# Kernel tuning notes

Measured on AMD Instinct MI355X. Metric: run time of the kernel, lower is better.

The kernel has to match this reference:

```python
import jax, jax.numpy as jnp
import numpy as np

FS, STRIDE, PAD = 3, 1, 1

def setup_inputs() -> dict:
    key = jax.random.key(0)
    k1, k2, k3 = jax.random.split(key, 3)
    N, C, H, W = 4, 256, 64, 64
    out_C = 256
    x = jax.random.normal(k1, (N, C, H, W), jnp.float32)
    # offset/mask conv params (original inits to 0 -> degenerate; use small random)
    offset_w = jax.random.normal(k2, (FS * FS * 3, C, FS, FS), jnp.float32) * 0.01
    offset_b = jnp.zeros((FS * FS * 3,), jnp.float32)
    # xavier_normal-like scale for dcn weight
    dcn_w = jax.random.normal(k3, (out_C, C, FS, FS), jnp.float32) * (1.0 / np.sqrt(C * FS * FS))
    return {"x": x, "offset_w": offset_w, "offset_b": offset_b, "dcn_w": dcn_w}

def _dcnv2(x, offset_w, offset_b, dcn_w):
    fs, stride, pad = FS, STRIDE, PAD
    N, C, H, W = x.shape
    out_C = dcn_w.shape[0]
    K2 = fs * fs
    om = jax.lax.conv_general_dilated(
        x, offset_w, (stride, stride), [(pad, pad), (pad, pad)],
        dimension_numbers=("NCHW", "OIHW", "NCHW")) + offset_b[None, :, None, None]
    Ho, Wo = om.shape[2], om.shape[3]
    offset = om[:, : 2 * K2].reshape(N, K2, 2, Ho, Wo)
    off_y, off_x = offset[:, :, 0], offset[:, :, 1]            # [N,K2,Ho,Wo]
    mask = jax.nn.sigmoid(om[:, 2 * K2:])                      # [N,K2,Ho,Wo]
    # base sampling grid: ori + kernel tap offset
    ky, kx = jnp.meshgrid(jnp.arange(fs), jnp.arange(fs), indexing="ij")
    ky = ky.reshape(K2).astype(jnp.float32)
    kx = kx.reshape(K2).astype(jnp.float32)
    base_y = (jnp.arange(Ho, dtype=jnp.float32) * stride - pad)[None, :, None] + ky[:, None, None]
    base_x = (jnp.arange(Wo, dtype=jnp.float32) * stride - pad)[None, None, :] + kx[:, None, None]
    h_im = base_y[None] + off_y                                # [N,K2,Ho,Wo]
    w_im = base_x[None] + off_x
    y0 = jnp.floor(h_im)
    x0 = jnp.floor(w_im)
    lh, lw = h_im - y0, w_im - x0
    xf = x.reshape(N, C, H * W)

    def gather(yi, xi):
        valid = (yi >= 0) & (yi <= H - 1) & (xi >= 0) & (xi <= W - 1)
        yc = jnp.clip(yi, 0, H - 1).astype(jnp.int32)
        xc = jnp.clip(xi, 0, W - 1).astype(jnp.int32)
        idx = (yc * W + xc).reshape(N, -1)
        v = jax.vmap(lambda img, ind: img[:, ind])(xf, idx)    # [N,C,K2*Ho*Wo]
        v = v.reshape(N, C, K2, Ho, Wo)
        return v * valid[:, None].astype(x.dtype)

    hh, hw = 1.0 - lh, 1.0 - lw
    sampled = ((hh * hw)[:, None] * gather(y0, x0)
               + (hh * lw)[:, None] * gather(y0, x0 + 1)
               + (lh * hw)[:, None] * gather(y0 + 1, x0)
               + (lh * lw)[:, None] * gather(y0 + 1, x0 + 1))  # [N,C,K2,Ho,Wo]
    sampled = sampled * mask[:, None]
    wk = dcn_w.reshape(out_C, C, K2)
    return jnp.einsum("nckhw,ock->nohw", sampled, wk)

def reference(x, offset_w, offset_b, dcn_w):
    return _dcnv2(x, offset_w, offset_b, dcn_w)
```

## Files before the change

kernel.cpp:

```cpp
#include <hip/hip_runtime.h>
#include <hip/hip_bf16.h>
#include <math.h>

#define NB     4
#define CIN    256
#define HH     64
#define WW     64
#define OUTC   256
#define K2     9
#define KTOT   2304
#define HWSZ   4096
#define NSTEPS 72
#define MTOT   16384


typedef __attribute__((ext_vector_type(4)))  float  floatx4;
typedef __attribute__((ext_vector_type(16))) float  floatx16;
typedef __attribute__((ext_vector_type(8)))  short  short8;
typedef __attribute__((ext_vector_type(4)))  short  short4v;
typedef __attribute__((ext_vector_type(4)))  int    intx4;

__device__ __forceinline__ unsigned short f2bf(float f) {
  union { float f; unsigned u; } v; v.f = f;
  unsigned r = v.u + 0x7FFF + ((v.u >> 16) & 1);
  return (unsigned short)(r >> 16);
}
__device__ __forceinline__ float b2f(unsigned short s) {
  union { unsigned u; float f; } v; v.u = ((unsigned)s) << 16;
  return v.f;
}
__device__ __forceinline__ float lo16f(int u) {
  union { int i; float f; } v; v.i = u << 16; return v.f;
}
__device__ __forceinline__ float hi16f(int u) {
  union { int i; float f; } v; v.i = u & 0xFFFF0000; return v.f;
}
__device__ __forceinline__ unsigned cvt_pk_bf16(float lo, float hi) {
  unsigned r;
  asm("v_cvt_pk_bf16_f32 %0, %1, %2" : "=v"(r) : "v"(lo), "v"(hi));
  return r;
}

__device__ __forceinline__ void pack8(const intx4& c0, const intx4& c1,
                                      const intx4& c2, const intx4& c3,
                                      const float4& w, unsigned short* dst) {
  intx4 o;
#pragma unroll
  for (int jj = 0; jj < 4; ++jj) {
    float v0 = w.x * lo16f(c0[jj]) + w.y * lo16f(c1[jj]) +
               w.z * lo16f(c2[jj]) + w.w * lo16f(c3[jj]);
    float v1 = w.x * hi16f(c0[jj]) + w.y * hi16f(c1[jj]) +
               w.z * hi16f(c2[jj]) + w.w * hi16f(c3[jj]);
    o[jj] = (int)cvt_pk_bf16(v0, v1);
  }
  *(intx4*)dst = o;
}

#define LDS_BARRIER() asm volatile("s_waitcnt lgkmcnt(0)\n\ts_barrier" ::: "memory")

#define WSM_BFRAG   0
#define WSM_B2FRAG  1179648
#define WSM_XT      (1179648 + 147456)
#define WSM_END     (WSM_XT + NB * HWSZ * CIN * 2)
#define WSF_BW      0
#define WSF_B2W     (KTOT * OUTC * 2)
#define WSF_OM      (WSF_B2W + KTOT * 32 * 2)
#define WSF_END     (WSF_OM + NB * 27 * HWSZ * 4)

__global__ __launch_bounds__(256) void prep_main_kernel(
    const float* __restrict__ dcn_w, const float* __restrict__ offw,
    const float* __restrict__ x,
    unsigned short* __restrict__ Bfrag, unsigned short* __restrict__ B2frag,
    unsigned short* __restrict__ xt) {
  int bid = blockIdx.x;
  int tid = threadIdx.x;
  if (bid < 256) {
    __shared__ unsigned short T[64 * 266];
    int img = bid >> 6, h = bid & 63;
    const float* xp = x + (size_t)img * CIN * HWSZ + h * 64;
    int w = tid & 63, cq = tid >> 6;
    for (int cb = 0; cb < 256; cb += 4) {
      int c = cb + cq;
      T[w * 266 + c] = f2bf(xp[(size_t)c * HWSZ + w]);
    }
    __syncthreads();
    int w2 = tid >> 2, cg = (tid & 3) << 6;
    unsigned short* o = xt + ((size_t)(img * 64 + h) * 64 + w2) * 256 + cg;
#pragma unroll
    for (int i = 0; i < 64; i += 8) {
      short8 v = *(short8*)&T[w2 * 266 + cg + i];
      *(short8*)(o + i) = v;
    }
  } else if (bid < 320) {
    __shared__ unsigned short W[4 * KTOT];
    int n0 = (bid - 256) * 4;
#pragma unroll
    for (int r = 0; r < 4; ++r)
      for (int c = tid; c < KTOT; c += 256)
        W[r * KTOT + c] = f2bf(dcn_w[(size_t)(n0 + r) * KTOT + c]);
    __syncthreads();
    for (int i = tid; i < 1152; i += 256) {
      int s16 = i >> 3, hf = (i >> 2) & 1, nl = i & 3;
      int n = n0 + nl;
      int lane = (hf << 5) + (n & 31);
      int e = (((s16 << 3) + (n >> 5)) << 6) + lane;
      int kb = (s16 << 4) + (hf << 3);
      short8 pk;
#pragma unroll
      for (int j = 0; j < 8; ++j) {
        int k = kb + j;
        pk[j] = (short)W[nl * KTOT + (k & 255) * 9 + (k >> 8)];
      }
      *(short8*)(Bfrag + (size_t)e * 8) = pk;
    }
  } else {
    __shared__ unsigned short W2[4 * KTOT];
    int n0 = (bid - 320) * 4;
#pragma unroll
    for (int r = 0; r < 4; ++r) {
      bool ok = (n0 + r) < 27;
      for (int c = tid; c < KTOT; c += 256)
        W2[r * KTOT + c] = ok ? f2bf(offw[(size_t)(n0 + r) * KTOT + c])
                              : (unsigned short)0;
    }
    __syncthreads();
    for (int i = tid; i < 1152; i += 256) {
      int s32 = i >> 4, qq = (i >> 2) & 3, nl = i & 3;
      int n = n0 + nl;
      int lane = (qq << 4) + (n & 15);
      int e = (((s32 << 1) + (n >> 4)) << 6) + lane;
      int kb = (s32 << 5) + (qq << 3);
      short8 pk;
#pragma unroll
      for (int j = 0; j < 8; ++j) {
        int k = kb + j;
        pk[j] = (short)W2[nl * KTOT + (k & 255) * 9 + (k >> 8)];
      }
      *(short8*)(B2frag + (size_t)e * 8) = pk;
    }
  }
}

__global__ __launch_bounds__(512, 2) void dcn_fused_kernel(
    const unsigned short* __restrict__ xt,
    const unsigned short* __restrict__ Bfrag,
    const unsigned short* __restrict__ B2frag,
    const float* __restrict__ ob, float* __restrict__ out) {
  __shared__ unsigned short Ald[4][520 * 8];
  __shared__ intx4  sOff[576];
  __shared__ float4 sWt[576];
  __shared__ float  omp[4 * 32 * 68];

  int braw = blockIdx.x;
  int bid  = ((braw & 7) << 5) + (braw >> 3);
  int img = bid >> 6, h = bid & 63;
  const unsigned short* xb = xt + (size_t)img * HWSZ * 256;

  int tid  = threadIdx.x;
  int lane = tid & 63, q = tid >> 6;
  int quad = lane >> 4, l15 = lane & 15;
  int l31  = lane & 31,  lh5 = lane >> 5;

  if (q < 4) {
    floatx4 cacc[4][2];
#pragma unroll
    for (int mt = 0; mt < 4; ++mt)
#pragma unroll
      for (int nt = 0; nt < 2; ++nt) cacc[mt][nt] = (floatx4){0.f, 0.f, 0.f, 0.f};
    short8 cpa[2][4];
    short8 cpb[2][2];

#define CONV_LOAD(I, SLOT)                                                     \
  {                                                                            \
    int s = q + (I) * 4;                                                       \
    int t = s >> 3;                                                            \
    int dy = t / 3 - 1, dx = t % 3 - 1;                                        \
    int y = h + dy;                                                            \
    int cb0 = ((s & 7) << 5) + (quad << 3);                                    \
    _Pragma("unroll")                                                          \
    for (int mt = 0; mt < 4; ++mt) {                                           \
      int xx = mt * 16 + l15 + dx;                                             \
      short8 v = {0, 0, 0, 0, 0, 0, 0, 0};                                     \
      if (((unsigned)y < 64u) && ((unsigned)xx < 64u))                         \
        v = *(const short8*)(xb + ((y * 64 + xx) << 8) + cb0);                 \
      cpa[SLOT][mt] = v;                                                       \
    }                                                                          \
    _Pragma("unroll")                                                          \
    for (int nt = 0; nt < 2; ++nt)                                             \
      cpb[SLOT][nt] = *(const short8*)(B2frag + (((s * 2 + nt) * 64 + lane) << 3)); \
  }

    CONV_LOAD(0, 0);
#pragma unroll 2
    for (int i = 0; i < 18; ++i) {
      int sl = i & 1;
      if (i < 17) CONV_LOAD(i + 1, sl ^ 1);
#pragma unroll
      for (int mt = 0; mt < 4; ++mt)
#pragma unroll
        for (int nt = 0; nt < 2; ++nt)
          cacc[mt][nt] = __builtin_amdgcn_mfma_f32_16x16x32_bf16(
              cpa[sl][mt], cpb[sl][nt], cacc[mt][nt], 0, 0, 0);
    }
#undef CONV_LOAD
#pragma unroll
    for (int mt = 0; mt < 4; ++mt)
#pragma unroll
      for (int nt = 0; nt < 2; ++nt) {
        int oc = nt * 16 + l15;
        float4 vv = make_float4(cacc[mt][nt][0], cacc[mt][nt][1],
                                cacc[mt][nt][2], cacc[mt][nt][3]);
        *(float4*)&omp[(q * 32 + oc) * 68 + mt * 16 + quad * 4] = vv;
      }
  }
  __syncthreads();

  for (int v = tid; v < 576; v += 512) {
    int w = v & 63, t = v >> 6;
    int ky = t / 3, kx = t % 3;
    float offy = omp[(0 * 32 + 2 * t) * 68 + w] + omp[(1 * 32 + 2 * t) * 68 + w] +
                 omp[(2 * 32 + 2 * t) * 68 + w] + omp[(3 * 32 + 2 * t) * 68 + w] +
                 ob[2 * t];
    float offx = omp[(0 * 32 + 2 * t + 1) * 68 + w] + omp[(1 * 32 + 2 * t + 1) * 68 + w] +
                 omp[(2 * 32 + 2 * t + 1) * 68 + w] + omp[(3 * 32 + 2 * t + 1) * 68 + w] +
                 ob[2 * t + 1];
    float mraw = omp[(0 * 32 + 18 + t) * 68 + w] + omp[(1 * 32 + 18 + t) * 68 + w] +
                 omp[(2 * 32 + 18 + t) * 68 + w] + omp[(3 * 32 + 18 + t) * 68 + w] +
                 ob[18 + t];
    float mv   = 1.0f / (1.0f + __expf(-mraw));
    float him  = (float)(h - 1 + ky) + offy;
    float wim  = (float)(w - 1 + kx) + offx;
    float y0f = floorf(him), x0f = floorf(wim);
    float lhf = him - y0f, lwf = wim - x0f;
    int y0 = (int)y0f, x0i = (int)x0f;
    bool vy0 = (y0 >= 0) && (y0 < HH);
    bool vy1 = (y0 + 1 >= 0) && (y0 + 1 < HH);
    bool vx0 = (x0i >= 0) && (x0i < WW);
    bool vx1 = (x0i + 1 >= 0) && (x0i + 1 < WW);
    float hh_ = 1.0f - lhf, hw_ = 1.0f - lwf;
    float4 wt;
    wt.x = (vy0 && vx0) ? hh_ * hw_ * mv : 0.0f;
    wt.y = (vy0 && vx1) ? hh_ * lwf * mv : 0.0f;
    wt.z = (vy1 && vx0) ? lhf * hw_ * mv : 0.0f;
    wt.w = (vy1 && vx1) ? lhf * lwf * mv : 0.0f;
    int y0c = min(max(y0, 0), 63), y1c = min(max(y0 + 1, 0), 63);
    int x0c = min(max(x0i, 0), 63), x1c = min(max(x0i + 1, 0), 63);
    intx4 ii = {(y0c * 64 + x0c) << 8, (y0c * 64 + x1c) << 8,
                (y1c * 64 + x0c) << 8, (y1c * 64 + x1c) << 8};
    sOff[v] = ii;
    sWt[v]  = wt;
  }

  floatx16 acc[2];
#pragma unroll
  for (int mt = 0; mt < 2; ++mt)
#pragma unroll
    for (int e = 0; e < 16; ++e) acc[mt][e] = 0.f;

  int sm  = tid >> 3;
  int chk = tid & 7;
  int wgran = (((chk >> 1) << 1) + (sm >> 5)) * 65 + ((chk & 1) << 5) + (sm & 31);

  short8 bfr[2][4];
  intx4  cr[2][4];
  float4 pwt[2];

  __syncthreads();

#pragma unroll
  for (int sub = 0; sub < 4; ++sub) {
    bfr[0][sub] = *(const short8*)(
        Bfrag + (((size_t)(0 + sub) * 8 + q) * 64 + lane) * 8);
    bfr[1][sub] = *(const short8*)(
        Bfrag + (((size_t)(4 + sub) * 8 + q) * 64 + lane) * 8);
  }
  {
    intx4 off = sOff[sm];
    float4 w0 = sWt[sm];
    {
      int cb = chk * 8;
      intx4 c0 = *(const intx4*)(xb + off.x + cb);
      intx4 c1 = *(const intx4*)(xb + off.y + cb);
      intx4 c2 = *(const intx4*)(xb + off.z + cb);
      intx4 c3 = *(const intx4*)(xb + off.w + cb);
      pack8(c0, c1, c2, c3, w0, &Ald[0][wgran * 8]);
    }
    {
      int cb = 64 + chk * 8;
      intx4 c0 = *(const intx4*)(xb + off.x + cb);
      intx4 c1 = *(const intx4*)(xb + off.y + cb);
      intx4 c2 = *(const intx4*)(xb + off.z + cb);
      intx4 c3 = *(const intx4*)(xb + off.w + cb);
      pack8(c0, c1, c2, c3, w0, &Ald[1][wgran * 8]);
    }
    {
      int cb = 128 + chk * 8;
      pwt[0] = w0;
      cr[0][0] = *(const intx4*)(xb + off.x + cb);
      cr[0][1] = *(const intx4*)(xb + off.y + cb);
      cr[0][2] = *(const intx4*)(xb + off.z + cb);
      cr[0][3] = *(const intx4*)(xb + off.w + cb);
    }
    {
      int cb = 192 + chk * 8;
      pwt[1] = w0;
      cr[1][0] = *(const intx4*)(xb + off.x + cb);
      cr[1][1] = *(const intx4*)(xb + off.y + cb);
      cr[1][2] = *(const intx4*)(xb + off.z + cb);
      cr[1][3] = *(const intx4*)(xb + off.w + cb);
    }
  }
  LDS_BARRIER();

#pragma unroll 2
  for (int S = 0; S < 18; ++S) {
    int s0 = 2 * S, s1 = s0 + 1;
    __builtin_amdgcn_s_setprio(1);
#pragma unroll
    for (int sub = 0; sub < 4; ++sub) {
      short8 a0 = *(short8*)&Ald[s0 & 3][((sub * 2 + 0) * 65 + lane) * 8];
      short8 a1 = *(short8*)&Ald[s0 & 3][((sub * 2 + 1) * 65 + lane) * 8];
      acc[0] = __builtin_amdgcn_mfma_f32_32x32x16_bf16(
          a0, bfr[0][sub], acc[0], 0, 0, 0);
      acc[1] = __builtin_amdgcn_mfma_f32_32x32x16_bf16(
          a1, bfr[0][sub], acc[1], 0, 0, 0);
    }
    __builtin_amdgcn_s_setprio(0);
    if (s0 + 2 < 36) {
      int s16b = (s0 + 2) * 4;
#pragma unroll
      for (int sub = 0; sub < 4; ++sub)
        bfr[0][sub] = *(const short8*)(
            Bfrag + (((size_t)(s16b + sub) * 8 + q) * 64 + lane) * 8);
      pack8(cr[0][0], cr[0][1], cr[0][2], cr[0][3], pwt[0],
            &Ald[(s0 + 2) & 3][wgran * 8]);
    }
    if (s0 + 4 < 36) {
      int s4 = s0 + 4, t4 = s4 >> 2;
      intx4 off = sOff[t4 * 64 + sm];
      pwt[0] = sWt[t4 * 64 + sm];
      int cb = (s4 & 3) * 64 + chk * 8;
      cr[0][0] = *(const intx4*)(xb + off.x + cb);
      cr[0][1] = *(const intx4*)(xb + off.y + cb);
      cr[0][2] = *(const intx4*)(xb + off.z + cb);
      cr[0][3] = *(const intx4*)(xb + off.w + cb);
    }
    __builtin_amdgcn_s_setprio(1);
#pragma unroll
    for (int sub = 0; sub < 4; ++sub) {
      short8 a0 = *(short8*)&Ald[s1 & 3][((sub * 2 + 0) * 65 + lane) * 8];
      short8 a1 = *(short8*)&Ald[s1 & 3][((sub * 2 + 1) * 65 + lane) * 8];
      acc[0] = __builtin_amdgcn_mfma_f32_32x32x16_bf16(
          a0, bfr[1][sub], acc[0], 0, 0, 0);
      acc[1] = __builtin_amdgcn_mfma_f32_32x32x16_bf16(
          a1, bfr[1][sub], acc[1], 0, 0, 0);
    }
    __builtin_amdgcn_s_setprio(0);
    if (s1 + 2 < 36) {
      int s16b = (s1 + 2) * 4;
#pragma unroll
      for (int sub = 0; sub < 4; ++sub)
        bfr[1][sub] = *(const short8*)(
            Bfrag + (((size_t)(s16b + sub) * 8 + q) * 64 + lane) * 8);
      pack8(cr[1][0], cr[1][1], cr[1][2], cr[1][3], pwt[1],
            &Ald[(s1 + 2) & 3][wgran * 8]);
    }
    if (s1 + 4 < 36) {
      int s4 = s1 + 4, t4 = s4 >> 2;
      intx4 off = sOff[t4 * 64 + sm];
      pwt[1] = sWt[t4 * 64 + sm];
      int cb = (s4 & 3) * 64 + chk * 8;
      cr[1][0] = *(const intx4*)(xb + off.x + cb);
      cr[1][1] = *(const intx4*)(xb + off.y + cb);
      cr[1][2] = *(const intx4*)(xb + off.z + cb);
      cr[1][3] = *(const intx4*)(xb + off.w + cb);
    }
    LDS_BARRIER();
  }

  int oc = q * 32 + l31;
#pragma unroll
  for (int mt = 0; mt < 2; ++mt) {
    float* obase = out + (((size_t)img * OUTC + oc) << 12) + h * 64 +
                   mt * 32 + lh5 * 4;
#pragma unroll
    for (int rg = 0; rg < 4; ++rg) {
      float4 vv = make_float4(acc[mt][rg * 4 + 0], acc[mt][rg * 4 + 1],
                              acc[mt][rg * 4 + 2], acc[mt][rg * 4 + 3]);
      *(float4*)(obase + rg * 8) = vv;
    }
  }
}

__global__ __launch_bounds__(256) void prep_fb_kernel(
    const float* __restrict__ dcn_w, const float* __restrict__ offw,
    unsigned short* __restrict__ Bw, unsigned short* __restrict__ B2w) {
  int oc = blockIdx.x;
  for (int k = threadIdx.x; k < KTOT; k += 256) {
    int t = k >> 8, c = k & 255;
    Bw[oc * KTOT + k] = f2bf(dcn_w[oc * KTOT + c * 9 + t]);
    if (oc < 32)
      B2w[oc * KTOT + k] = (oc < 27) ? f2bf(offw[oc * KTOT + c * 9 + t])
                                     : (unsigned short)0;
  }
}

__global__ __launch_bounds__(256) void conv_offset_kernel(
    const float* __restrict__ x, const unsigned short* __restrict__ B2w,
    const float* __restrict__ ob, float* __restrict__ om) {
  __shared__ unsigned short A_lds[64 * 40];
  __shared__ unsigned short B_lds[32 * 40];
  int bid = blockIdx.x;
  int n = bid >> 6, h = bid & 63;
  int tid = threadIdx.x, lane = tid & 63, q = tid >> 6;
  const float* xn = x + n * (CIN * HWSZ);
  floatx4 acc0 = {0.f, 0.f, 0.f, 0.f}, acc1 = {0.f, 0.f, 0.f, 0.f};
  int w = tid & 63, cg = tid >> 6, ocb = tid >> 3, part = tid & 7;
  for (int s = 0; s < NSTEPS; ++s) {
    int t = s >> 3, c0 = (s & 7) << 5;
    int dy = t / 3 - 1, dx = t % 3 - 1;
    __syncthreads();
    {
      int y = h + dy, xx = w + dx;
      bool inb = ((unsigned)y < 64u) && ((unsigned)xx < 64u);
      const float* xb = xn + (c0 + cg * 8) * HWSZ + y * 64 + xx;
      short8 pk;
#pragma unroll
      for (int j = 0; j < 8; ++j) { float v = inb ? xb[j * HWSZ] : 0.0f; pk[j] = (short)f2bf(v); }
      *(short8*)&A_lds[w * 40 + cg * 8] = pk;
    }
    { const unsigned short* bp = B2w + ocb * KTOT + (t << 8) + c0 + part * 4;
      *(short4v*)&B_lds[ocb * 40 + part * 4] = *(const short4v*)bp; }
    __syncthreads();
    int fr = (lane >> 4) * 8;
    short8 af  = *(short8*)&A_lds[(q * 16 + (lane & 15)) * 40 + fr];
    short8 bf0 = *(short8*)&B_lds[((lane & 15)) * 40 + fr];
    short8 bf1 = *(short8*)&B_lds[(16 + (lane & 15)) * 40 + fr];
    acc0 = __builtin_amdgcn_mfma_f32_16x16x32_bf16(af, bf0, acc0, 0, 0, 0);
    acc1 = __builtin_amdgcn_mfma_f32_16x16x32_bf16(af, bf1, acc1, 0, 0, 0);
  }
  int g = lane >> 4;
#pragma unroll
  for (int nt = 0; nt < 2; ++nt) {
    floatx4 a = nt ? acc1 : acc0;
    int oc = nt * 16 + (lane & 15);
    if (oc < 27) {
      float bias = ob[oc];
#pragma unroll
      for (int r = 0; r < 4; ++r) {
        int wm = q * 16 + g * 4 + r;
        float val = a[r] + bias;
        if (oc >= 18) val = 1.0f / (1.0f + __expf(-val));
        om[((n * 27 + oc) << 12) + h * 64 + wm] = val;
      }
    }
  }
}

__global__ __launch_bounds__(256) void dcn_main_kernel(
    const float* __restrict__ x, const float* __restrict__ om,
    const unsigned short* __restrict__ Bw, float* __restrict__ out) {
  __shared__ unsigned short A_lds[32 * 40];
  __shared__ unsigned short B_lds[256 * 40];
  __shared__ int    sY[288];
  __shared__ int    sX[288];
  __shared__ float4 sW[288];
  int bid = blockIdx.x;
  int n = bid >> 7, rem = bid & 127, h = rem >> 1, w0 = (rem & 1) << 5;
  int tid = threadIdx.x, lane = tid & 63, q = tid >> 6;
  const float* xn  = x + n * (CIN * HWSZ);
  const float* omn = om + n * (27 * HWSZ);
  for (int v = tid; v < 288; v += 256) {
    int m = v & 31, t = v >> 5;
    int ky = t / 3, kx = t % 3;
    int wg = w0 + m, sp = h * 64 + wg;
    float offy = omn[(2 * t) * HWSZ + sp];
    float offx = omn[(2 * t + 1) * HWSZ + sp];
    float mv   = omn[(18 + t) * HWSZ + sp];
    float him = (float)(h - 1 + ky) + offy;
    float wim = (float)(wg - 1 + kx) + offx;
    float y0f = floorf(him), x0f = floorf(wim);
    float lh = him - y0f, lw = wim - x0f;
    int y0 = (int)y0f, x0i = (int)x0f;
    bool vy0 = (y0 >= 0) && (y0 < HH), vy1 = (y0 + 1 >= 0) && (y0 + 1 < HH);
    bool vx0 = (x0i >= 0) && (x0i < WW), vx1 = (x0i + 1 >= 0) && (x0i + 1 < WW);
    float hh_ = 1.0f - lh, hw_ = 1.0f - lw;
    float4 wt;
    wt.x = (vy0 && vx0) ? hh_ * hw_ * mv : 0.0f;
    wt.y = (vy0 && vx1) ? hh_ * lw  * mv : 0.0f;
    wt.z = (vy1 && vx0) ? lh  * hw_ * mv : 0.0f;
    wt.w = (vy1 && vx1) ? lh  * lw  * mv : 0.0f;
    sY[v] = y0; sX[v] = x0i; sW[v] = wt;
  }
  floatx4 acc[2][4];
#pragma unroll
  for (int mi = 0; mi < 2; ++mi)
#pragma unroll
    for (int nj = 0; nj < 4; ++nj) acc[mi][nj] = (floatx4){0.f, 0.f, 0.f, 0.f};
  int m = tid & 31, cg = tid >> 5, n0 = q * 64;
  for (int s = 0; s < NSTEPS; ++s) {
    int t = s >> 3, c0 = (s & 7) << 5;
    __syncthreads();
    {
      int p = t * 32 + m;
      int y0 = sY[p], x0i = sX[p];
      float4 wt = sW[p];
      int y0c = min(max(y0, 0), 63), y1c = min(max(y0 + 1, 0), 63);
      int x0c = min(max(x0i, 0), 63), x1c = min(max(x0i + 1, 0), 63);
      int i00 = y0c * 64 + x0c, i01 = y0c * 64 + x1c;
      int i10 = y1c * 64 + x0c, i11 = y1c * 64 + x1c;
      const float* xb = xn + (c0 + cg * 4) * HWSZ;
      short4v pk;
#pragma unroll
      for (int j = 0; j < 4; ++j) {
        const float* xc = xb + j * HWSZ;
        float v = wt.x * xc[i00] + wt.y * xc[i01] + wt.z * xc[i10] + wt.w * xc[i11];
        pk[j] = (short)f2bf(v);
      }
      *(short4v*)&A_lds[m * 40 + cg * 4] = pk;
    }
    {
      const short8* bp = (const short8*)(Bw + tid * KTOT + (t << 8) + c0);
      short8 b0 = bp[0], b1 = bp[1], b2 = bp[2], b3 = bp[3];
      short8* dst = (short8*)&B_lds[tid * 40];
      dst[0] = b0; dst[1] = b1; dst[2] = b2; dst[3] = b3;
    }
    __syncthreads();
    int fr = (lane >> 4) * 8;
    short8 a0 = *(short8*)&A_lds[((lane & 15)) * 40 + fr];
    short8 a1 = *(short8*)&A_lds[(16 + (lane & 15)) * 40 + fr];
#pragma unroll
    for (int nj = 0; nj < 4; ++nj) {
      short8 bfp = *(short8*)&B_lds[(n0 + nj * 16 + (lane & 15)) * 40 + fr];
      acc[0][nj] = __builtin_amdgcn_mfma_f32_16x16x32_bf16(a0, bfp, acc[0][nj], 0, 0, 0);
      acc[1][nj] = __builtin_amdgcn_mfma_f32_16x16x32_bf16(a1, bfp, acc[1][nj], 0, 0, 0);
    }
  }
  int g = lane >> 4;
#pragma unroll
  for (int mi = 0; mi < 2; ++mi) {
    int wm = w0 + mi * 16 + g * 4;
#pragma unroll
    for (int nj = 0; nj < 4; ++nj) {
      int oc = n0 + nj * 16 + (lane & 15);
      float4 vv = make_float4(acc[mi][nj][0], acc[mi][nj][1],
                              acc[mi][nj][2], acc[mi][nj][3]);
      *(float4*)&out[((n * OUTC + oc) << 12) + h * 64 + wm] = vv;
    }
  }
}

extern "C" void kernel_launch(void* const* d_in, const int* in_sizes, int n_in,
                              void* d_out, int out_size, void* d_ws, size_t ws_size,
                              hipStream_t stream) {
  const float* x     = (const float*)d_in[0];
  const float* offw  = (const float*)d_in[1];
  const float* ob    = (const float*)d_in[2];
  const float* dcn_w = (const float*)d_in[3];
  float* out = (float*)d_out;

  if (ws_size >= (size_t)WSM_END) {
    unsigned short* Bfrag  = (unsigned short*)((char*)d_ws + WSM_BFRAG);
    unsigned short* B2frag = (unsigned short*)((char*)d_ws + WSM_B2FRAG);
    unsigned short* xtb    = (unsigned short*)((char*)d_ws + WSM_XT);
    prep_main_kernel<<<328, 256, 0, stream>>>(dcn_w, offw, x, Bfrag, B2frag, xtb);
    dcn_fused_kernel<<<256, 512, 0, stream>>>(xtb, Bfrag, B2frag, ob, out);
  } else {
    unsigned short* Bw  = (unsigned short*)((char*)d_ws + WSF_BW);
    unsigned short* B2w = (unsigned short*)((char*)d_ws + WSF_B2W);
    float*          omb = (float*)((char*)d_ws + WSF_OM);
    prep_fb_kernel<<<256, 256, 0, stream>>>(dcn_w, offw, Bw, B2w);
    conv_offset_kernel<<<NB * HH, 256, 0, stream>>>(x, B2w, ob, omb);
    dcn_main_kernel<<<NB * HH * 2, 256, 0, stream>>>(x, omb, Bw, out);
  }
}
```

Measured before the change: 130.7 us.

## Split fused DCN blocks into half-row tiles and flatten weight-prep kernel

The fused deformable-conv kernel now processes half an output row (32 pixels) per block instead of a full row, doubling the grid to 512 blocks so every CU gets work and LDS use per block shrinks. Only the first 256 threads produce gathered A tiles, and each wave issues one 32x32 MFMA chain instead of two. The weight-fragment prep drops its LDS staging and has each thread build one fragment straight from global memory over more blocks. The trade-off is that B fragments and the offset-conv halo are loaded twice per row, and half the threads sit idle during packing.

Result: slower. 133.8 us (+2.3%).

```diff
diff --git a/kernel.cpp b/kernel.cpp
--- a/kernel.cpp
+++ b/kernel.cpp
@@ -91,53 +91,31 @@
       short8 v = *(short8*)&T[w2 * 266 + cg + i];
       *(short8*)(o + i) = v;
     }
-  } else if (bid < 320) {
-    __shared__ unsigned short W[4 * KTOT];
-    int n0 = (bid - 256) * 4;
-#pragma unroll
-    for (int r = 0; r < 4; ++r)
-      for (int c = tid; c < KTOT; c += 256)
-        W[r * KTOT + c] = f2bf(dcn_w[(size_t)(n0 + r) * KTOT + c]);
-    __syncthreads();
-    for (int i = tid; i < 1152; i += 256) {
-      int s16 = i >> 3, hf = (i >> 2) & 1, nl = i & 3;
-      int n = n0 + nl;
-      int lane = (hf << 5) + (n & 31);
-      int e = (((s16 << 3) + (n >> 5)) << 6) + lane;
-      int kb = (s16 << 4) + (hf << 3);
-      short8 pk;
-#pragma unroll
-      for (int j = 0; j < 8; ++j) {
-        int k = kb + j;
-        pk[j] = (short)W[nl * KTOT + (k & 255) * 9 + (k >> 8)];
-      }
-      *(short8*)(Bfrag + (size_t)e * 8) = pk;
-    }
+  } else if (bid < 544) {
+    int e = (bid - 256) * 256 + tid;
+    int lane = e & 63, nt = (e >> 6) & 7, s16 = e >> 9;
+    int n = nt * 32 + (lane & 31);
+    int kb = s16 * 16 + ((lane >> 5) << 3);
+    short8 pk;
+#pragma unroll
+    for (int j = 0; j < 8; ++j) {
+      int k = kb + j;
+      pk[j] = (short)f2bf(dcn_w[n * KTOT + (k & 255) * 9 + (k >> 8)]);
+    }
+    *(short8*)(Bfrag + (size_t)e * 8) = pk;
   } else {
-    __shared__ unsigned short W2[4 * KTOT];
-    int n0 = (bid - 320) * 4;
-#pragma unroll
-    for (int r = 0; r < 4; ++r) {
-      bool ok = (n0 + r) < 27;
-      for (int c = tid; c < KTOT; c += 256)
-        W2[r * KTOT + c] = ok ? f2bf(offw[(size_t)(n0 + r) * KTOT + c])
-                              : (unsigned short)0;
-    }
-    __syncthreads();
-    for (int i = tid; i < 1152; i += 256) {
-      int s32 = i >> 4, qq = (i >> 2) & 3, nl = i & 3;
-      int n = n0 + nl;
-      int lane = (qq << 4) + (n & 15);
-      int e = (((s32 << 1) + (n >> 4)) << 6) + lane;
-      int kb = (s32 << 5) + (qq << 3);
-      short8 pk;
-#pragma unroll
-      for (int j = 0; j < 8; ++j) {
-        int k = kb + j;
-        pk[j] = (short)W2[nl * KTOT + (k & 255) * 9 + (k >> 8)];
-      }
-      *(short8*)(B2frag + (size_t)e * 8) = pk;
-    }
+    int e = (bid - 544) * 256 + tid;
+    int lane = e & 63, nt = (e >> 6) & 1, s32 = e >> 7;
+    int n = nt * 16 + (lane & 15);
+    int kb = s32 * 32 + ((lane >> 4) << 3);
+    short8 pk;
+#pragma unroll
+    for (int j = 0; j < 8; ++j) {
+      int k = kb + j;
+      pk[j] = (n < 27) ? (short)f2bf(offw[n * KTOT + (k & 255) * 9 + (k >> 8)])
+                       : (short)0;
+    }
+    *(short8*)(B2frag + (size_t)e * 8) = pk;
   }
 }
 
@@ -146,14 +124,16 @@
     const unsigned short* __restrict__ Bfrag,
     const unsigned short* __restrict__ B2frag,
     const float* __restrict__ ob, float* __restrict__ out) {
-  __shared__ unsigned short Ald[4][520 * 8];
-  __shared__ intx4  sOff[576];
-  __shared__ float4 sWt[576];
-  __shared__ float  omp[4 * 32 * 68];
+  __shared__ unsigned short Ald[4][260 * 8];
+  __shared__ intx4  sOff[288];
+  __shared__ float4 sWt[288];
+  __shared__ float  omp[4 * 32 * 36];
 
   int braw = blockIdx.x;
-  int bid  = ((braw & 7) << 5) + (braw >> 3);
-  int img = bid >> 6, h = bid & 63;
+  int bid  = ((braw & 7) << 6) + (braw >> 3);
+  int rowid = bid >> 1, half = bid & 1;
+  int img = rowid >> 6, h = rowid & 63;
+  int w0 = half << 5;
   const unsigned short* xb = xt + (size_t)img * HWSZ * 256;
 
   int tid  = threadIdx.x;
@@ -162,12 +142,12 @@
   int l31  = lane & 31,  lh5 = lane >> 5;
 
   if (q < 4) {
-    floatx4 cacc[4][2];
-#pragma unroll
-    for (int mt = 0; mt < 4; ++mt)
+    floatx4 cacc[2][2];
+#pragma unroll
+    for (int mt = 0; mt < 2; ++mt)
 #pragma unroll
       for (int nt = 0; nt < 2; ++nt) cacc[mt][nt] = (floatx4){0.f, 0.f, 0.f, 0.f};
-    short8 cpa[2][4];
+    short8 cpa[2][2];
     short8 cpb[2][2];
 
 #define CONV_LOAD(I, SLOT)                                                     \
@@ -178,8 +158,8 @@
     int y = h + dy;                                                            \
     int cb0 = ((s & 7) << 5) + (quad << 3);                                    \
     _Pragma("unroll")                                                          \
-    for (int mt = 0; mt < 4; ++mt) {                                           \
-      int xx = mt * 16 + l15 + dx;                                             \
+    for (int mt = 0; mt < 2; ++mt) {                                           \
+      int xx = w0 + mt * 16 + l15 + dx;                                        \
       short8 v = {0, 0, 0, 0, 0, 0, 0, 0};                                     \
       if (((unsigned)y < 64u) && ((unsigned)xx < 64u))                         \
         v = *(const short8*)(xb + ((y * 64 + xx) << 8) + cb0);                 \
@@ -196,7 +176,7 @@
       int sl = i & 1;
       if (i < 17) CONV_LOAD(i + 1, sl ^ 1);
 #pragma unroll
-      for (int mt = 0; mt < 4; ++mt)
+      for (int mt = 0; mt < 2; ++mt)
 #pragma unroll
         for (int nt = 0; nt < 2; ++nt)
           cacc[mt][nt] = __builtin_amdgcn_mfma_f32_16x16x32_bf16(
@@ -204,32 +184,34 @@
     }
 #undef CONV_LOAD
 #pragma unroll
-    for (int mt = 0; mt < 4; ++mt)
+    for (int mt = 0; mt < 2; ++mt)
 #pragma unroll
       for (int nt = 0; nt < 2; ++nt) {
         int oc = nt * 16 + l15;
         float4 vv = make_float4(cacc[mt][nt][0], cacc[mt][nt][1],
                                 cacc[mt][nt][2], cacc[mt][nt][3]);
-        *(float4*)&omp[(q * 32 + oc) * 68 + mt * 16 + quad * 4] = vv;
+        *(float4*)&omp[(q * 32 + oc) * 36 + mt * 16 + quad * 4] = vv;
       }
   }
   __syncthreads();
 
-  for (int v = tid; v < 576; v += 512) {
-    int w = v & 63, t = v >> 6;
+  if (tid < 288) {
+    int v = tid;
+    int w = v & 31, t = v >> 5;
+    int wg = w0 + w;
     int ky = t / 3, kx = t % 3;
-    float offy = omp[(0 * 32 + 2 * t) * 68 + w] + omp[(1 * 32 + 2 * t) * 68 + w] +
-                 omp[(2 * 32 + 2 * t) * 68 + w] + omp[(3 * 32 + 2 * t) * 68 + w] +
+    float offy = omp[(0 * 32 + 2 * t) * 36 + w] + omp[(1 * 32 + 2 * t) * 36 + w] +
+                 omp[(2 * 32 + 2 * t) * 36 + w] + omp[(3 * 32 + 2 * t) * 36 + w] +
                  ob[2 * t];
-    float offx = omp[(0 * 32 + 2 * t + 1) * 68 + w] + omp[(1 * 32 + 2 * t + 1) * 68 + w] +
-                 omp[(2 * 32 + 2 * t + 1) * 68 + w] + omp[(3 * 32 + 2 * t + 1) * 68 + w] +
+    float offx = omp[(0 * 32 + 2 * t + 1) * 36 + w] + omp[(1 * 32 + 2 * t + 1) * 36 + w] +
+                 omp[(2 * 32 + 2 * t + 1) * 36 + w] + omp[(3 * 32 + 2 * t + 1) * 36 + w] +
                  ob[2 * t + 1];
-    float mraw = omp[(0 * 32 + 18 + t) * 68 + w] + omp[(1 * 32 + 18 + t) * 68 + w] +
-                 omp[(2 * 32 + 18 + t) * 68 + w] + omp[(3 * 32 + 18 + t) * 68 + w] +
+    float mraw = omp[(0 * 32 + 18 + t) * 36 + w] + omp[(1 * 32 + 18 + t) * 36 + w] +
+                 omp[(2 * 32 + 18 + t) * 36 + w] + omp[(3 * 32 + 18 + t) * 36 + w] +
                  ob[18 + t];
     float mv   = 1.0f / (1.0f + __expf(-mraw));
     float him  = (float)(h - 1 + ky) + offy;
-    float wim  = (float)(w - 1 + kx) + offx;
+    float wim  = (float)(wg - 1 + kx) + offx;
     float y0f = floorf(him), x0f = floorf(wim);
     float lhf = him - y0f, lwf = wim - x0f;
     int y0 = (int)y0f, x0i = (int)x0f;
@@ -251,15 +233,14 @@
     sWt[v]  = wt;
   }
 
-  floatx16 acc[2];
-#pragma unroll
-  for (int mt = 0; mt < 2; ++mt)
-#pragma unroll
-    for (int e = 0; e < 16; ++e) acc[mt][e] = 0.f;
-
-  int sm  = tid >> 3;
+  floatx16 acc;
+#pragma unroll
+  for (int e = 0; e < 16; ++e) acc[e] = 0.f;
+
+  int sm  = (tid >> 3) & 31;
   int chk = tid & 7;
-  int wgran = (((chk >> 1) << 1) + (sm >> 5)) * 65 + ((chk & 1) << 5) + (sm & 31);
+  int wgran = (chk >> 1) * 65 + ((chk & 1) << 5) + sm;
+  bool producer = (tid < 256);
 
   short8 bfr[2][4];
   intx4  cr[2][4];
@@ -274,16 +255,16 @@
     bfr[1][sub] = *(const short8*)(
         Bfrag + (((size_t)(4 + sub) * 8 + q) * 64 + lane) * 8);
   }
-  {
+  if (producer) {
     intx4 off = sOff[sm];
-    float4 w0 = sWt[sm];
+    float4 wgt = sWt[sm];
     {
       int cb = chk * 8;
       intx4 c0 = *(const intx4*)(xb + off.x + cb);
       intx4 c1 = *(const intx4*)(xb + off.y + cb);
       intx4 c2 = *(const intx4*)(xb + off.z + cb);
       intx4 c3 = *(const intx4*)(xb + off.w + cb);
-      pack8(c0, c1, c2, c3, w0, &Ald[0][wgran * 8]);
+      pack8(c0, c1, c2, c3, wgt, &Ald[0][wgran * 8]);
     }
     {
       int cb = 64 + chk * 8;
@@ -291,11 +272,11 @@
       intx4 c1 = *(const intx4*)(xb + off.y + cb);
       intx4 c2 = *(const intx4*)(xb + off.z + cb);
       intx4 c3 = *(const intx4*)(xb + off.w + cb);
-      pack8(c0, c1, c2, c3, w0, &Ald[1][wgran * 8]);
+      pack8(c0, c1, c2, c3, wgt, &Ald[1][wgran * 8]);
     }
     {
       int cb = 128 + chk * 8;
-      pwt[0] = w0;
+      pwt[0] = wgt;
       cr[0][0] = *(const intx4*)(xb + off.x + cb);
       cr[0][1] = *(const intx4*)(xb + off.y + cb);
       cr[0][2] = *(const intx4*)(xb + off.z + cb);
@@ -303,7 +284,7 @@
     }
     {
       int cb = 192 + chk * 8;
-      pwt[1] = w0;
+      pwt[1] = wgt;
       cr[1][0] = *(const intx4*)(xb + off.x + cb);
       cr[1][1] = *(const intx4*)(xb + off.y + cb);
       cr[1][2] = *(const intx4*)(xb + off.z + cb);
@@ -318,12 +299,8 @@
     __builtin_amdgcn_s_setprio(1);
 #pragma unroll
     for (int sub = 0; sub < 4; ++sub) {
-      short8 a0 = *(short8*)&Ald[s0 & 3][((sub * 2 + 0) * 65 + lane) * 8];
-      short8 a1 = *(short8*)&Ald[s0 & 3][((sub * 2 + 1) * 65 + lane) * 8];
-      acc[0] = __builtin_amdgcn_mfma_f32_32x32x16_bf16(
-          a0, bfr[0][sub], acc[0], 0, 0, 0);
-      acc[1] = __builtin_amdgcn_mfma_f32_32x32x16_bf16(
-          a1, bfr[0][sub], acc[1], 0, 0, 0);
+      short8 a = *(short8*)&Ald[s0 & 3][(sub * 65 + lane) * 8];
+      acc = __builtin_amdgcn_mfma_f32_32x32x16_bf16(a, bfr[0][sub], acc, 0, 0, 0);
     }
     __builtin_amdgcn_s_setprio(0);
     if (s0 + 2 < 36) {
@@ -332,13 +309,14 @@
       for (int sub = 0; sub < 4; ++sub)
         bfr[0][sub] = *(const short8*)(
             Bfrag + (((size_t)(s16b + sub) * 8 + q) * 64 + lane) * 8);
-      pack8(cr[0][0], cr[0][1], cr[0][2], cr[0][3], pwt[0],
-            &Ald[(s0 + 2) & 3][wgran * 8]);
-    }
-    if (s0 + 4 < 36) {
+      if (producer)
+        pack8(cr[0][0], cr[0][1], cr[0][2], cr[0][3], pwt[0],
+              &Ald[(s0 + 2) & 3][wgran * 8]);
+    }
+    if (producer && (s0 + 4 < 36)) {
       int s4 = s0 + 4, t4 = s4 >> 2;
-      intx4 off = sOff[t4 * 64 + sm];
-      pwt[0] = sWt[t4 * 64 + sm];
+      intx4 off = sOff[t4 * 32 + sm];
+      pwt[0] = sWt[t4 * 32 + sm];
       int cb = (s4 & 3) * 64 + chk * 8;
       cr[0][0] = *(const intx4*)(xb + off.x + cb);
       cr[0][1] = *(const intx4*)(xb + off.y + cb);
@@ -348,12 +326,8 @@
     __builtin_amdgcn_s_setprio(1);
 #pragma unroll
     for (int sub = 0; sub < 4; ++sub) {
-      short8 a0 = *(short8*)&Ald[s1 & 3][((sub * 2 + 0) * 65 + lane) * 8];
-      short8 a1 = *(short8*)&Ald[s1 & 3][((sub * 2 + 1) * 65 + lane) * 8];
-      acc[0] = __builtin_amdgcn_mfma_f32_32x32x16_bf16(
-          a0, bfr[1][sub], acc[0], 0, 0, 0);
-      acc[1] = __builtin_amdgcn_mfma_f32_32x32x16_bf16(
-          a1, bfr[1][sub], acc[1], 0, 0, 0);
+      short8 a = *(short8*)&Ald[s1 & 3][(sub * 65 + lane) * 8];
+      acc = __builtin_amdgcn_mfma_f32_32x32x16_bf16(a, bfr[1][sub], acc, 0, 0, 0);
     }
     __builtin_amdgcn_s_setprio(0);
     if (s1 + 2 < 36) {
@@ -362,13 +336,14 @@
       for (int sub = 0; sub < 4; ++sub)
         bfr[1][sub] = *(const short8*)(
             Bfrag + (((size_t)(s16b + sub) * 8 + q) * 64 + lane) * 8);
-      pack8(cr[1][0], cr[1][1], cr[1][2], cr[1][3], pwt[1],
-            &Ald[(s1 + 2) & 3][wgran * 8]);
-    }
-    if (s1 + 4 < 36) {
+      if (producer)
+        pack8(cr[1][0], cr[1][1], cr[1][2], cr[1][3], pwt[1],
+              &Ald[(s1 + 2) & 3][wgran * 8]);
+    }
+    if (producer && (s1 + 4 < 36)) {
       int s4 = s1 + 4, t4 = s4 >> 2;
-      intx4 off = sOff[t4 * 64 + sm];
-      pwt[1] = sWt[t4 * 64 + sm];
+      intx4 off = sOff[t4 * 32 + sm];
+      pwt[1] = sWt[t4 * 32 + sm];
       int cb = (s4 & 3) * 64 + chk * 8;
       cr[1][0] = *(const intx4*)(xb + off.x + cb);
       cr[1][1] = *(const intx4*)(xb + off.y + cb);
@@ -379,16 +354,12 @@
   }
 
   int oc = q * 32 + l31;
-#pragma unroll
-  for (int mt = 0; mt < 2; ++mt) {
-    float* obase = out + (((size_t)img * OUTC + oc) << 12) + h * 64 +
-                   mt * 32 + lh5 * 4;
-#pragma unroll
-    for (int rg = 0; rg < 4; ++rg) {
-      float4 vv = make_float4(acc[mt][rg * 4 + 0], acc[mt][rg * 4 + 1],
-                              acc[mt][rg * 4 + 2], acc[mt][rg * 4 + 3]);
-      *(float4*)(obase + rg * 8) = vv;
-    }
+  float* obase = out + (((size_t)img * OUTC + oc) << 12) + h * 64 + w0 + lh5 * 4;
+#pragma unroll
+  for (int rg = 0; rg < 4; ++rg) {
+    float4 vv = make_float4(acc[rg * 4 + 0], acc[rg * 4 + 1],
+                            acc[rg * 4 + 2], acc[rg * 4 + 3]);
+    *(float4*)(obase + rg * 8) = vv;
   }
 }
 
@@ -563,8 +534,8 @@
     unsigned short* Bfrag  = (unsigned short*)((char*)d_ws + WSM_BFRAG);
     unsigned short* B2frag = (unsigned short*)((char*)d_ws + WSM_B2FRAG);
     unsigned short* xtb    = (unsigned short*)((char*)d_ws + WSM_XT);
-    prep_main_kernel<<<328, 256, 0, stream>>>(dcn_w, offw, x, Bfrag, B2frag, xtb);
-    dcn_fused_kernel<<<256, 512, 0, stream>>>(xtb, Bfrag, B2frag, ob, out);
+    prep_main_kernel<<<580, 256, 0, stream>>>(dcn_w, offw, x, Bfrag, B2frag, xtb);
+    dcn_fused_kernel<<<512, 512, 0, stream>>>(xtb, Bfrag, B2frag, ob, out);
   } else {
     unsigned short* Bw  = (unsigned short*)((char*)d_ws + WSF_BW);
     unsigned short* B2w = (unsigned short*)((char*)d_ws + WSF_B2W);
```

## Stagger wave roles in main loop and parallelize weight-fragment prep

Applied to the files above, without the earlier changes.

The weight-fragment prep blocks are rewritten so each thread produces one packed fragment directly from global memory instead of staging rows in shared memory. The grid grows from 328 to 580 blocks to cover this finer split. In the fused kernel's main loop, half the waves (q<4) now do gather/pack work before their MFMAs while the other half do MFMAs first, so matrix and memory work overlap across waves. The per-thread prep reads are strided rather than coalesced, and reordering pack before MFMA within a step relies on the ring buffer depth being enough to avoid hazards.

Result: faster. 123.4 us (-5.6%).

```diff
diff --git a/kernel.cpp b/kernel.cpp
--- a/kernel.cpp
+++ b/kernel.cpp
@@ -91,53 +91,31 @@
       short8 v = *(short8*)&T[w2 * 266 + cg + i];
       *(short8*)(o + i) = v;
     }
-  } else if (bid < 320) {
-    __shared__ unsigned short W[4 * KTOT];
-    int n0 = (bid - 256) * 4;
-#pragma unroll
-    for (int r = 0; r < 4; ++r)
-      for (int c = tid; c < KTOT; c += 256)
-        W[r * KTOT + c] = f2bf(dcn_w[(size_t)(n0 + r) * KTOT + c]);
-    __syncthreads();
-    for (int i = tid; i < 1152; i += 256) {
-      int s16 = i >> 3, hf = (i >> 2) & 1, nl = i & 3;
-      int n = n0 + nl;
-      int lane = (hf << 5) + (n & 31);
-      int e = (((s16 << 3) + (n >> 5)) << 6) + lane;
-      int kb = (s16 << 4) + (hf << 3);
-      short8 pk;
-#pragma unroll
-      for (int j = 0; j < 8; ++j) {
-        int k = kb + j;
-        pk[j] = (short)W[nl * KTOT + (k & 255) * 9 + (k >> 8)];
-      }
-      *(short8*)(Bfrag + (size_t)e * 8) = pk;
-    }
+  } else if (bid < 544) {
+    int e = (bid - 256) * 256 + tid;
+    int lane = e & 63, nt = (e >> 6) & 7, s16 = e >> 9;
+    int n = nt * 32 + (lane & 31);
+    int kb = s16 * 16 + ((lane >> 5) << 3);
+    short8 pk;
+#pragma unroll
+    for (int j = 0; j < 8; ++j) {
+      int k = kb + j;
+      pk[j] = (short)f2bf(dcn_w[n * KTOT + (k & 255) * 9 + (k >> 8)]);
+    }
+    *(short8*)(Bfrag + (size_t)e * 8) = pk;
   } else {
-    __shared__ unsigned short W2[4 * KTOT];
-    int n0 = (bid - 320) * 4;
-#pragma unroll
-    for (int r = 0; r < 4; ++r) {
-      bool ok = (n0 + r) < 27;
-      for (int c = tid; c < KTOT; c += 256)
-        W2[r * KTOT + c] = ok ? f2bf(offw[(size_t)(n0 + r) * KTOT + c])
-                              : (unsigned short)0;
-    }
-    __syncthreads();
-    for (int i = tid; i < 1152; i += 256) {
-      int s32 = i >> 4, qq = (i >> 2) & 3, nl = i & 3;
-      int n = n0 + nl;
-      int lane = (qq << 4) + (n & 15);
-      int e = (((s32 << 1) + (n >> 4)) << 6) + lane;
-      int kb = (s32 << 5) + (qq << 3);
-      short8 pk;
-#pragma unroll
-      for (int j = 0; j < 8; ++j) {
-        int k = kb + j;
-        pk[j] = (short)W2[nl * KTOT + (k & 255) * 9 + (k >> 8)];
-      }
-      *(short8*)(B2frag + (size_t)e * 8) = pk;
-    }
+    int e = (bid - 544) * 256 + tid;
+    int lane = e & 63, nt = (e >> 6) & 1, s32 = e >> 7;
+    int n = nt * 16 + (lane & 15);
+    int kb = s32 * 32 + ((lane >> 4) << 3);
+    short8 pk;
+#pragma unroll
+    for (int j = 0; j < 8; ++j) {
+      int k = kb + j;
+      pk[j] = (n < 27) ? (short)f2bf(offw[n * KTOT + (k & 255) * 9 + (k >> 8)])
+                       : (short)0;
+    }
+    *(short8*)(B2frag + (size_t)e * 8) = pk;
   }
 }
 
@@ -312,71 +290,71 @@
   }
   LDS_BARRIER();
 
-#pragma unroll 2
+#define MFMA_STEP(SX, P)                                                       \
+  {                                                                            \
+    __builtin_amdgcn_s_setprio(1);                                             \
+    _Pragma("unroll")                                                          \
+    for (int sub = 0; sub < 4; ++sub) {                                        \
+      short8 a0 = *(short8*)&Ald[(SX) & 3][((sub * 2 + 0) * 65 + lane) * 8];   \
+      short8 a1 = *(short8*)&Ald[(SX) & 3][((sub * 2 + 1) * 65 + lane) * 8];   \
+      acc[0] = __builtin_amdgcn_mfma_f32_32x32x16_bf16(                        \
+          a0, bfr[P][sub], acc[0], 0, 0, 0);                                   \
+      acc[1] = __builtin_amdgcn_mfma_f32_32x32x16_bf16(                        \
+          a1, bfr[P][sub], acc[1], 0, 0, 0);                                   \
+    }                                                                          \
+    __builtin_amdgcn_s_setprio(0);                                             \
+  }
+#define BLOAD_STEP(SX, P)                                                      \
+  if ((SX) + 2 < 36) {                                                         \
+    int s16b = ((SX) + 2) * 4;                                                 \
+    _Pragma("unroll")                                                          \
+    for (int sub = 0; sub < 4; ++sub)                                          \
+      bfr[P][sub] = *(const short8*)(                                          \
+          Bfrag + (((size_t)(s16b + sub) * 8 + q) * 64 + lane) * 8);           \
+  }
+#define PACK_STEP(SX, P)                                                       \
+  if ((SX) + 2 < 36)                                                           \
+    pack8(cr[P][0], cr[P][1], cr[P][2], cr[P][3], pwt[P],                      \
+          &Ald[((SX) + 2) & 3][wgran * 8]);
+#define CLOAD_STEP(SX, P)                                                      \
+  if ((SX) + 4 < 36) {                                                         \
+    int s4 = (SX) + 4, t4 = s4 >> 2;                                           \
+    intx4 off = sOff[t4 * 64 + sm];                                            \
+    pwt[P] = sWt[t4 * 64 + sm];                                                \
+    int cb = (s4 & 3) * 64 + chk * 8;                                          \
+    cr[P][0] = *(const intx4*)(xb + off.x + cb);                               \
+    cr[P][1] = *(const intx4*)(xb + off.y + cb);                               \
+    cr[P][2] = *(const intx4*)(xb + off.z + cb);                               \
+    cr[P][3] = *(const intx4*)(xb + off.w + cb);                               \
+  }
+
   for (int S = 0; S < 18; ++S) {
     int s0 = 2 * S, s1 = s0 + 1;
-    __builtin_amdgcn_s_setprio(1);
-#pragma unroll
-    for (int sub = 0; sub < 4; ++sub) {
-      short8 a0 = *(short8*)&Ald[s0 & 3][((sub * 2 + 0) * 65 + lane) * 8];
-      short8 a1 = *(short8*)&Ald[s0 & 3][((sub * 2 + 1) * 65 + lane) * 8];
-      acc[0] = __builtin_amdgcn_mfma_f32_32x32x16_bf16(
-          a0, bfr[0][sub], acc[0], 0, 0, 0);
-      acc[1] = __builtin_amdgcn_mfma_f32_32x32x16_bf16(
-          a1, bfr[0][sub], acc[1], 0, 0, 0);
-    }
-    __builtin_amdgcn_s_setprio(0);
-    if (s0 + 2 < 36) {
-      int s16b = (s0 + 2) * 4;
-#pragma unroll
-      for (int sub = 0; sub < 4; ++sub)
-        bfr[0][sub] = *(const short8*)(
-            Bfrag + (((size_t)(s16b + sub) * 8 + q) * 64 + lane) * 8);
-      pack8(cr[0][0], cr[0][1], cr[0][2], cr[0][3], pwt[0],
-            &Ald[(s0 + 2) & 3][wgran * 8]);
-    }
-    if (s0 + 4 < 36) {
-      int s4 = s0 + 4, t4 = s4 >> 2;
-      intx4 off = sOff[t4 * 64 + sm];
-      pwt[0] = sWt[t4 * 64 + sm];
-      int cb = (s4 & 3) * 64 + chk * 8;
-      cr[0][0] = *(const intx4*)(xb + off.x + cb);
-      cr[0][1] = *(const intx4*)(xb + off.y + cb);
-      cr[0][2] = *(const intx4*)(xb + off.z + cb);
-      cr[0][3] = *(const intx4*)(xb + off.w + cb);
-    }
-    __builtin_amdgcn_s_setprio(1);
-#pragma unroll
-    for (int sub = 0; sub < 4; ++sub) {
-      short8 a0 = *(short8*)&Ald[s1 & 3][((sub * 2 + 0) * 65 + lane) * 8];
-      short8 a1 = *(short8*)&Ald[s1 & 3][((sub * 2 + 1) * 65 + lane) * 8];
-      acc[0] = __builtin_amdgcn_mfma_f32_32x32x16_bf16(
-          a0, bfr[1][sub], acc[0], 0, 0, 0);
-      acc[1] = __builtin_amdgcn_mfma_f32_32x32x16_bf16(
-          a1, bfr[1][sub], acc[1], 0, 0, 0);
-    }
-    __builtin_amdgcn_s_setprio(0);
-    if (s1 + 2 < 36) {
-      int s16b = (s1 + 2) * 4;
-#pragma unroll
-      for (int sub = 0; sub < 4; ++sub)
-        bfr[1][sub] = *(const short8*)(
-            Bfrag + (((size_t)(s16b + sub) * 8 + q) * 64 + lane) * 8);
-      pack8(cr[1][0], cr[1][1], cr[1][2], cr[1][3], pwt[1],
-            &Ald[(s1 + 2) & 3][wgran * 8]);
-    }
-    if (s1 + 4 < 36) {
-      int s4 = s1 + 4, t4 = s4 >> 2;
-      intx4 off = sOff[t4 * 64 + sm];
-      pwt[1] = sWt[t4 * 64 + sm];
-      int cb = (s4 & 3) * 64 + chk * 8;
-      cr[1][0] = *(const intx4*)(xb + off.x + cb);
-      cr[1][1] = *(const intx4*)(xb + off.y + cb);
-      cr[1][2] = *(const intx4*)(xb + off.z + cb);
-      cr[1][3] = *(const intx4*)(xb + off.w + cb);
+    if (q < 4) {
+      PACK_STEP(s0, 0);
+      CLOAD_STEP(s0, 0);
+      PACK_STEP(s1, 1);
+      CLOAD_STEP(s1, 1);
+      MFMA_STEP(s0, 0);
+      BLOAD_STEP(s0, 0);
+      MFMA_STEP(s1, 1);
+      BLOAD_STEP(s1, 1);
+    } else {
+      MFMA_STEP(s0, 0);
+      BLOAD_STEP(s0, 0);
+      MFMA_STEP(s1, 1);
+      BLOAD_STEP(s1, 1);
+      PACK_STEP(s0, 0);
+      CLOAD_STEP(s0, 0);
+      PACK_STEP(s1, 1);
+      CLOAD_STEP(s1, 1);
     }
     LDS_BARRIER();
   }
+#undef MFMA_STEP
+#undef BLOAD_STEP
+#undef PACK_STEP
+#undef CLOAD_STEP
 
   int oc = q * 32 + l31;
 #pragma unroll
@@ -563,7 +541,7 @@
     unsigned short* Bfrag  = (unsigned short*)((char*)d_ws + WSM_BFRAG);
     unsigned short* B2frag = (unsigned short*)((char*)d_ws + WSM_B2FRAG);
     unsigned short* xtb    = (unsigned short*)((char*)d_ws + WSM_XT);
-    prep_main_kernel<<<328, 256, 0, stream>>>(dcn_w, offw, x, Bfrag, B2frag, xtb);
+    prep_main_kernel<<<580, 256, 0, stream>>>(dcn_w, offw, x, Bfrag, B2frag, xtb);
     dcn_fused_kernel<<<256, 512, 0, stream>>>(xtb, Bfrag, B2frag, ob, out);
   } else {
     unsigned short* Bw  = (unsigned short*)((char*)d_ws + WSF_BW);
```

## Parallelize weight fragment packing per element and use packed FMA in bilinear pack

Applied to the files above, without the earlier changes.

The weight-prep blocks no longer stage four output rows in LDS. Each thread now builds one 8-element MFMA B fragment directly from global memory, and the grid grows from 328 to 580 blocks so the weight packing runs across many more workgroups. The aim is to shorten the prep kernel's long serial tail. Separately, the bilinear interpolation in pack8 uses v_pk_fma_f32 to compute the low and high bf16 halves together, which roughly halves the FMA instruction count. The cost is strided, uncoalesced global reads of the weights, each converted once per thread.

New measurement: 120.6 us, median of 2. 1.08x faster.

```diff
diff --git a/kernel.cpp b/kernel.cpp
--- a/kernel.cpp
+++ b/kernel.cpp
@@ -14,6 +14,7 @@
 #define MTOT   16384
 
 
+typedef __attribute__((ext_vector_type(2)))  float  floatx2;
 typedef __attribute__((ext_vector_type(4)))  float  floatx4;
 typedef __attribute__((ext_vector_type(16))) float  floatx16;
 typedef __attribute__((ext_vector_type(8)))  short  short8;
@@ -40,18 +41,29 @@
   asm("v_cvt_pk_bf16_f32 %0, %1, %2" : "=v"(r) : "v"(lo), "v"(hi));
   return r;
 }
+__device__ __forceinline__ floatx2 pk_fma(floatx2 a, floatx2 b, floatx2 c) {
+  floatx2 d;
+  asm("v_pk_fma_f32 %0, %1, %2, %3" : "=v"(d) : "v"(a), "v"(b), "v"(c));
+  return d;
+}
 
 __device__ __forceinline__ void pack8(const intx4& c0, const intx4& c1,
                                       const intx4& c2, const intx4& c3,
                                       const float4& w, unsigned short* dst) {
+  floatx2 w0 = {w.x, w.x}, w1 = {w.y, w.y}, w2 = {w.z, w.z}, w3 = {w.w, w.w};
   intx4 o;
 #pragma unroll
   for (int jj = 0; jj < 4; ++jj) {
-    float v0 = w.x * lo16f(c0[jj]) + w.y * lo16f(c1[jj]) +
-               w.z * lo16f(c2[jj]) + w.w * lo16f(c3[jj]);
-    float v1 = w.x * hi16f(c0[jj]) + w.y * hi16f(c1[jj]) +
-               w.z * hi16f(c2[jj]) + w.w * hi16f(c3[jj]);
-    o[jj] = (int)cvt_pk_bf16(v0, v1);
+    floatx2 p0 = {lo16f(c0[jj]), hi16f(c0[jj])};
+    floatx2 p1 = {lo16f(c1[jj]), hi16f(c1[jj])};
+    floatx2 p2 = {lo16f(c2[jj]), hi16f(c2[jj])};
+    floatx2 p3 = {lo16f(c3[jj]), hi16f(c3[jj])};
+    floatx2 a = {0.f, 0.f};
+    a = pk_fma(w0, p0, a);
+    a = pk_fma(w1, p1, a);
+    a = pk_fma(w2, p2, a);
+    a = pk_fma(w3, p3, a);
+    o[jj] = (int)cvt_pk_bf16(a[0], a[1]);
   }
   *(intx4*)dst = o;
 }
@@ -91,53 +103,31 @@
       short8 v = *(short8*)&T[w2 * 266 + cg + i];
       *(short8*)(o + i) = v;
     }
-  } else if (bid < 320) {
-    __shared__ unsigned short W[4 * KTOT];
-    int n0 = (bid - 256) * 4;
-#pragma unroll
-    for (int r = 0; r < 4; ++r)
-      for (int c = tid; c < KTOT; c += 256)
-        W[r * KTOT + c] = f2bf(dcn_w[(size_t)(n0 + r) * KTOT + c]);
-    __syncthreads();
-    for (int i = tid; i < 1152; i += 256) {
-      int s16 = i >> 3, hf = (i >> 2) & 1, nl = i & 3;
-      int n = n0 + nl;
-      int lane = (hf << 5) + (n & 31);
-      int e = (((s16 << 3) + (n >> 5)) << 6) + lane;
-      int kb = (s16 << 4) + (hf << 3);
-      short8 pk;
-#pragma unroll
-      for (int j = 0; j < 8; ++j) {
-        int k = kb + j;
-        pk[j] = (short)W[nl * KTOT + (k & 255) * 9 + (k >> 8)];
-      }
-      *(short8*)(Bfrag + (size_t)e * 8) = pk;
-    }
+  } else if (bid < 544) {
+    int e = (bid - 256) * 256 + tid;
+    int lane = e & 63, nt = (e >> 6) & 7, s16 = e >> 9;
+    int n = nt * 32 + (lane & 31);
+    int kb = s16 * 16 + ((lane >> 5) << 3);
+    short8 pk;
+#pragma unroll
+    for (int j = 0; j < 8; ++j) {
+      int k = kb + j;
+      pk[j] = (short)f2bf(dcn_w[n * KTOT + (k & 255) * 9 + (k >> 8)]);
+    }
+    *(short8*)(Bfrag + (size_t)e * 8) = pk;
   } else {
-    __shared__ unsigned short W2[4 * KTOT];
-    int n0 = (bid - 320) * 4;
-#pragma unroll
-    for (int r = 0; r < 4; ++r) {
-      bool ok = (n0 + r) < 27;
-      for (int c = tid; c < KTOT; c += 256)
-        W2[r * KTOT + c] = ok ? f2bf(offw[(size_t)(n0 + r) * KTOT + c])
-                              : (unsigned short)0;
-    }
-    __syncthreads();
-    for (int i = tid; i < 1152; i += 256) {
-      int s32 = i >> 4, qq = (i >> 2) & 3, nl = i & 3;
-      int n = n0 + nl;
-      int lane = (qq << 4) + (n & 15);
-      int e = (((s32 << 1) + (n >> 4)) << 6) + lane;
-      int kb = (s32 << 5) + (qq << 3);
-      short8 pk;
-#pragma unroll
-      for (int j = 0; j < 8; ++j) {
-        int k = kb + j;
-        pk[j] = (short)W2[nl * KTOT + (k & 255) * 9 + (k >> 8)];
-      }
-      *(short8*)(B2frag + (size_t)e * 8) = pk;
-    }
+    int e = (bid - 544) * 256 + tid;
+    int lane = e & 63, nt = (e >> 6) & 1, s32 = e >> 7;
+    int n = nt * 16 + (lane & 15);
+    int kb = s32 * 32 + ((lane >> 4) << 3);
+    short8 pk;
+#pragma unroll
+    for (int j = 0; j < 8; ++j) {
+      int k = kb + j;
+      pk[j] = (n < 27) ? (short)f2bf(offw[n * KTOT + (k & 255) * 9 + (k >> 8)])
+                       : (short)0;
+    }
+    *(short8*)(B2frag + (size_t)e * 8) = pk;
   }
 }
 
@@ -563,7 +553,7 @@
     unsigned short* Bfrag  = (unsigned short*)((char*)d_ws + WSM_BFRAG);
     unsigned short* B2frag = (unsigned short*)((char*)d_ws + WSM_B2FRAG);
     unsigned short* xtb    = (unsigned short*)((char*)d_ws + WSM_XT);
-    prep_main_kernel<<<328, 256, 0, stream>>>(dcn_w, offw, x, Bfrag, B2frag, xtb);
+    prep_main_kernel<<<580, 256, 0, stream>>>(dcn_w, offw, x, Bfrag, B2frag, xtb);
     dcn_fused_kernel<<<256, 512, 0, stream>>>(xtb, Bfrag, B2frag, ob, out);
   } else {
     unsigned short* Bw  = (unsigned short*)((char*)d_ws + WSF_BW);
```
